# Performance work log

Measured on AMD Instinct MI355X. Metric: run time of the kernel, lower is better.

The kernel has to match this reference:

```python
import jax, jax.numpy as jnp
import numpy as np

# Dimensions
B, C, H, W, M, ND = 2, 16, 128, 128, 9, 9  # batch, feat, height, width, views, disparities
MC = M * C          # 144 channels after view stacking
HID = 18            # hidden channels in attention branches
OUT = 150           # output_dim of conv_last
EPS = 1e-5          # BatchNorm eps
PAD = 16            # max |d*(u-4)| = 4*4


def _conv3d(x, w, b, pad):
    # x: [N, Cin, D, H, W]; w: [Cout, Cin, kd, kh, kw]
    y = jax.lax.conv_general_dilated(
        x, w, window_strides=(1, 1, 1), padding=[(pad, pad)] * 3,
        dimension_numbers=('NCDHW', 'OIDHW', 'NCDHW'))
    return y + b.reshape(1, -1, 1, 1, 1)


def _bn(x, g, b, m, v):
    # eval-mode BatchNorm3d with running stats
    sh = (1, -1, 1, 1, 1)
    return (x - m.reshape(sh)) * (g * jax.lax.rsqrt(v + EPS)).reshape(sh) + b.reshape(sh)


def _cost_volume(x):
    # x: [B,C,H,W,M] -> cost volume [B,M,C,H,W,ND] (mode '0d': v=4, u=view index).
    # affine_grid(align_corners=False) theta=[[1,0,2d(u-4)/W],[0,1,0]] + bilinear
    # grid_sample is an EXACT integer horizontal shift: out[h,w] = in[h, w + d*(u-4)]
    # with zero padding outside the image.
    xv = jnp.transpose(x, (4, 0, 1, 2, 3))                      # [M,B,C,H,W]
    xp = jnp.pad(xv, ((0, 0), (0, 0), (0, 0), (PAD, PAD), (PAD, PAD)))
    vols = []
    for d in range(-4, 5):
        views = [xp[m, :, :, PAD:PAD + H, PAD + d * (m - 4):PAD + d * (m - 4) + W]
                 for m in range(M)]
        vols.append(jnp.stack(views, axis=1))                   # [B,M,C,H,W]
    return jnp.stack(vols, axis=-1)                             # [B,M,C,H,W,ND]


def setup_inputs() -> dict:
    key = jax.random.key(0)
    ks = jax.random.split(key, 32)
    f = lambda k, shape, s=0.05: (jax.random.normal(k, shape, jnp.float32) * s)
    inp = {
        'x': jax.random.normal(ks[0], (B, C, H, W, M), jnp.float32),
        # local attention branch
        'la_w1': f(ks[1], (HID, MC, 3, 3, 3)), 'la_b1': f(ks[2], (HID,)),
        'la_g1': 1.0 + f(ks[3], (HID,)), 'la_beta1': f(ks[4], (HID,)),
        'la_m1': f(ks[5], (HID,)), 'la_v1': 1.0 + 0.1 * jax.random.uniform(ks[6], (HID,), jnp.float32),
        'la_w2': f(ks[7], (M, HID, 3, 3, 3)), 'la_b2': f(ks[8], (M,)),
        'la_g2': 1.0 + f(ks[9], (M,)), 'la_beta2': f(ks[10], (M,)),
        'la_m2': f(ks[11], (M,)), 'la_v2': 1.0 + 0.1 * jax.random.uniform(ks[12], (M,), jnp.float32),
        # global attention branch
        'ga_w1': f(ks[13], (HID, MC, 3, 3, 3)), 'ga_b1': f(ks[14], (HID,)),
        'ga_g1': 1.0 + f(ks[15], (HID,)), 'ga_beta1': f(ks[16], (HID,)),
        'ga_m1': f(ks[17], (HID,)), 'ga_v1': 1.0 + 0.1 * jax.random.uniform(ks[18], (HID,), jnp.float32),
        'ga_w2': f(ks[19], (M, HID, 3, 3, 3)), 'ga_b2': f(ks[20], (M,)),
        'ga_g2': 1.0 + f(ks[21], (M,)), 'ga_beta2': f(ks[22], (M,)),
        'ga_m2': f(ks[23], (M,)), 'ga_v2': 1.0 + 0.1 * jax.random.uniform(ks[24], (M,), jnp.float32),
        # conv_last (1x1x1)
        'cl_w': f(ks[25], (OUT, MC, 1, 1, 1)), 'cl_b': f(ks[26], (OUT,)),
    }
    return inp


def reference(x, la_w1, la_b1, la_g1, la_beta1, la_m1, la_v1,
              la_w2, la_b2, la_g2, la_beta2, la_m2, la_v2,
              ga_w1, ga_b1, ga_g1, ga_beta1, ga_m1, ga_v1,
              ga_w2, ga_b2, ga_g2, ga_beta2, ga_m2, ga_v2,
              cl_w, cl_b):
    cv = _cost_volume(x)                                        # [B,M,C,H,W,ND]
    xr = cv.reshape(B, MC, H, W, ND)                            # [B,144,H,W,9]
    # local attention
    h = jax.nn.relu(_bn(_conv3d(xr, la_w1, la_b1, 1), la_g1, la_beta1, la_m1, la_v1))
    x_l = _bn(_conv3d(h, la_w2, la_b2, 1), la_g2, la_beta2, la_m2, la_v2)   # [B,9,H,W,9]
    # global attention (adaptive avg pool to 1x1x1 then same conv stack)
    p = jnp.mean(xr, axis=(2, 3, 4), keepdims=True)             # [B,144,1,1,1]
    g = jax.nn.relu(_bn(_conv3d(p, ga_w1, ga_b1, 1), ga_g1, ga_beta1, ga_m1, ga_v1))
    x_g = _bn(_conv3d(g, ga_w2, ga_b2, 1), ga_g2, ga_beta2, ga_m2, ga_v2)   # [B,9,1,1,1]
    wei = jax.nn.sigmoid(x_l + x_g).reshape(B, M, 1, H, W, ND)
    out = _conv3d((wei * cv).reshape(B, MC, H, W, ND), cl_w, cl_b, 0)       # [B,150,H,W,9]
    return out.reshape(B, -1, H, W, ND)
```

## Files before the change

kernel.cpp:

```cpp
#include <hip/hip_runtime.h>
#include <hip/hip_bf16.h>
#include <cstddef>

#define B_ 2
#define C_ 16
#define H_ 128
#define W_ 128
#define M_ 9
#define ND_ 9
#define MC_ 144
#define HID_ 18
#define OUT_ 150
#define GOC_ 152
#define EPS_ 1e-5f

#define OFF_P     0
#define OFF_XG    512
#define OFF_W1F   1024
#define OFF_B1F   71040
#define OFF_W2F   71104
#define OFF_B2F   75520
#define OFF_CLWT  75584
#define OFF_F     98304
#define OFF_HBUF  18069504
#define OFF_WEI   23377920
#define OFF_GB_BYTES (98304ull*4ull)

__global__ __launch_bounds__(256) void k_pool(const float* __restrict__ x,
                                              float* __restrict__ ws) {
  int bid = blockIdx.x;
  int z   = blockIdx.y;
  int b = bid / MC_, mc = bid % MC_;
  int m = mc / C_, c = mc % C_;
  int sm = m - 4;
  const float* xb = x + (size_t)(b*C_ + c)*H_*W_*M_;
  float acc = 0.f;
  int i0 = z * (H_*W_*ND_/8);
  int i1 = i0 + (H_*W_*ND_/8);
  for (int idx = i0 + (int)threadIdx.x; idx < i1; idx += 256) {
    int w = idx & 127;
    int t = idx >> 7;
    int d = t % 9;
    int h = t / 9;
    int wc = w + (d - 4)*sm;
    if (wc >= 0 && wc < W_) acc += xb[(h*W_ + wc)*M_ + m];
  }
  __shared__ float red[256];
  red[threadIdx.x] = acc;
  __syncthreads();
  for (int s = 128; s > 0; s >>= 1) {
    if ((int)threadIdx.x < s) red[threadIdx.x] += red[threadIdx.x + s];
    __syncthreads();
  }
  if (threadIdx.x == 0)
    atomicAdd(&ws[OFF_P + b*MC_ + mc], red[0] * (1.f/(float)(H_*W_*ND_)));
}

__global__ __launch_bounds__(256) void k_repack(
    const float* __restrict__ w1, const float* __restrict__ b1,
    const float* __restrict__ g1, const float* __restrict__ be1,
    const float* __restrict__ m1, const float* __restrict__ v1,
    const float* __restrict__ w2, const float* __restrict__ b2,
    const float* __restrict__ g2, const float* __restrict__ be2,
    const float* __restrict__ m2, const float* __restrict__ v2,
    const float* __restrict__ clw, float* __restrict__ ws) {
  int id = blockIdx.x*256 + threadIdx.x;
  if (id < 69984) {
    int o   = id % 18;
    int kdd = (id/18) % 3;
    int kh  = (id/54) % 3;
    int kw  = (id/162) % 3;
    int mc  = id/486;
    float s = g1[o] / sqrtf(v1[o] + EPS_);
    ws[OFF_W1F + id] = w1[(o*MC_ + mc)*27 + kh*9 + kw*3 + kdd] * s;
    return;
  }
  id -= 69984;
  if (id < 18) {
    float s = g1[id]/sqrtf(v1[id]+EPS_);
    ws[OFF_B1F + id] = (b1[id]-m1[id])*s + be1[id];
    return;
  }
  id -= 18;
  if (id < 4374) {
    int i = id % 9, tap = (id/9) % 27, c = id/243;
    float s = g2[i]/sqrtf(v2[i]+EPS_);
    ws[OFF_W2F + id] = w2[(i*HID_ + c)*27 + tap] * s;
    return;
  }
  id -= 4374;
  if (id < 9) {
    float s = g2[id]/sqrtf(v2[id]+EPS_);
    ws[OFF_B2F + id] = (b2[id]-m2[id])*s + be2[id];
    return;
  }
  id -= 9;
  if (id < 21600) {
    int oc = id % OUT_, mc = id / OUT_;
    ws[OFF_CLWT + id] = clw[oc*MC_ + mc];
  }
}

__global__ __launch_bounds__(64) void k_ga(
    const float* __restrict__ gw1, const float* __restrict__ gb1,
    const float* __restrict__ gg1, const float* __restrict__ gbe1,
    const float* __restrict__ gm1, const float* __restrict__ gv1,
    const float* __restrict__ gw2, const float* __restrict__ gb2,
    const float* __restrict__ gg2, const float* __restrict__ gbe2,
    const float* __restrict__ gm2, const float* __restrict__ gv2,
    float* __restrict__ ws) {
  __shared__ float gl[B_*HID_];
  int t = threadIdx.x;
  if (t < B_*HID_) {
    int b = t / HID_, j = t % HID_;
    float acc = gb1[j];
    for (int ch = 0; ch < MC_; ch++)
      acc += gw1[(j*MC_ + ch)*27 + 13] * ws[OFF_P + b*MC_ + ch];
    float s = gg1[j]/sqrtf(gv1[j]+EPS_);
    gl[t] = fmaxf((acc - gm1[j])*s + gbe1[j], 0.f);
  }
  __syncthreads();
  if (t < B_*M_) {
    int b = t / M_, i = t % M_;
    float acc = gb2[i];
    for (int j = 0; j < HID_; j++)
      acc += gw2[(i*HID_ + j)*27 + 13] * gl[b*HID_ + j];
    float s = gg2[i]/sqrtf(gv2[i]+EPS_);
    ws[OFF_XG + b*M_ + i] = (acc - gm2[i])*s + gbe2[i];
  }
}

__global__ __launch_bounds__(256) void k_F(const float* __restrict__ x,
                                           float* __restrict__ ws) {
  int h0 = blockIdx.x * 4;
  int m  = blockIdx.y;
  int b  = blockIdx.z;
  __shared__ float xt[C_*132*6];
  for (int e = threadIdx.x; e < C_*132*6; e += 256) {
    int hh = e % 6;
    int cc = (e/6) % 132;
    int c  = e / 792;
    int row = h0 - 1 + hh;
    int col = cc - 2;
    float v = 0.f;
    if (row >= 0 && row < H_ && col >= 0 && col < W_)
      v = x[(((size_t)(b*C_ + c)*H_ + row)*W_ + col)*M_ + m];
    xt[e] = v;
  }
  __syncthreads();
  const float* w1f = ws + OFF_W1F;
  float* Fb = ws + OFF_F + (size_t)(b*M_ + m)*3*H_*130*20;
  for (int pp = threadIdx.x; pp < 130*18; pp += 256) {
    int o   = pp % 18;
    int wpp = pp / 18;
    float acc[3][4] = {};
    for (int c = 0; c < C_; c++) {
      int wb = (m*C_ + c)*486 + o;
      #pragma unroll
      for (int kw = 0; kw < 3; kw++) {
        const float* xp = xt + (c*132 + wpp + kw)*6;
        float xv[6];
        #pragma unroll
        for (int q = 0; q < 6; q++) xv[q] = xp[q];
        const float* wp = w1f + wb + kw*162;
        #pragma unroll
        for (int kh = 0; kh < 3; kh++)
          #pragma unroll
          for (int kdd = 0; kdd < 3; kdd++) {
            float wv = wp[kh*54 + kdd*18];
            #pragma unroll
            for (int hh = 0; hh < 4; hh++)
              acc[kdd][hh] += wv * xv[hh + kh];
          }
      }
    }
    #pragma unroll
    for (int kdd = 0; kdd < 3; kdd++)
      #pragma unroll
      for (int hh = 0; hh < 4; hh++)
        Fb[(((size_t)kdd*H_ + (h0+hh))*130 + wpp)*20 + o] = acc[kdd][hh];
  }
}

__global__ __launch_bounds__(576) void k_comb1(const float* __restrict__ x,
                                               float* __restrict__ ws) {
  const int h = blockIdx.x;
  const int b = blockIdx.y;
  const int t = threadIdx.x;
  const int d    = t >> 6;
  const int lane = t & 63;

  __shared__ float fs[3*2730];
  __shared__ float xe[7776];
  __shared__ float corr[9][2][18];

  const int iA = t, iB = t + 576, iC = t + 1152, iD = t + 1728;
  const bool vD = (iD < 1950);
  const int kA = iA/650, rA_ = iA%650;
  const int kB = iB/650, rB_ = iB%650;
  const int kC = iC/650, rC_ = iC%650;
  const int kD = vD ? iD/650 : 0, rD_ = vD ? iD%650 : 0;
  const int gA = kA*332800 + h*2600 + rA_*4;
  const int gB = kB*332800 + h*2600 + rB_*4;
  const int gC = kC*332800 + h*2600 + rC_*4;
  const int gD = kD*332800 + h*2600 + rD_*4;
  const int lA = kA*2730 + (rA_/5)*21 + (rA_%5)*4;
  const int lB = kB*2730 + (rB_/5)*21 + (rB_%5)*4;
  const int lC = kC*2730 + (rC_/5)*21 + (rC_%5)*4;
  const int lD = kD*2730 + (rD_/5)*21 + (rD_%5)*4;

  size_t mb = (size_t)OFF_F + (size_t)(b*9 + 0)*998400;
  float4 rA = *(const float4*)(ws + mb + gA);
  float4 rB = *(const float4*)(ws + mb + gB);
  float4 rC = *(const float4*)(ws + mb + gC);
  float4 rD = vD ? *(const float4*)(ws + mb + gD) : make_float4(0.f,0.f,0.f,0.f);

  for (int e = t; e < 7776; e += 576) {
    int c    = e & 15;
    int kh   = (e >> 4) % 3;
    int dp   = (e / 48) % 9;
    int edge = (e / 432) & 1;
    int m    = e / 864;
    int row = h + kh - 1;
    int col = edge ? 128 + (dp - 4)*(m - 4) : (dp - 4)*(m - 4) - 1;
    float v = 0.f;
    if ((unsigned)row < 128u && (unsigned)col < 128u)
      v = x[(((size_t)(b*C_ + c)*H_ + row)*W_ + col)*M_ + m];
    xe[e] = v;
  }
  __syncthreads();

  if (t < 324) {
    int o    = t % 18;
    int edge = (t / 18) & 1;
    int dd   = t / 36;
    int kwe  = edge ? 2 : 0;
    const float* w1b = ws + OFF_W1F + kwe*162 + o;
    float s = 0.f;
    for (int m = 0; m < 9; m++) {
      #pragma unroll
      for (int kdd = 0; kdd < 3; kdd++) {
        int dp = dd + kdd - 1;
        if (dp < 0 || dp >= 9) continue;
        const float* xp = xe + ((m*2 + edge)*9 + dp)*48;
        const float* wp = w1b + m*7776 + kdd*18;
        for (int c = 0; c < 16; c++) {
          #pragma unroll
          for (int kh = 0; kh < 3; kh++)
            s += wp[c*486 + kh*54] * xp[kh*16 + c];
        }
      }
    }
    corr[dd][edge][o] = s;
  }

  float acc0[18], acc1[18];
  #pragma unroll
  for (int o = 0; o < 18; o++) {
    float bz = ws[OFF_B1F + o];
    acc0[o] = bz; acc1[o] = bz;
  }

  __syncthreads();

  for (int m = 0; m < 9; m++) {
    fs[lA+0]=rA.x; fs[lA+1]=rA.y; fs[lA+2]=rA.z; fs[lA+3]=rA.w;
    fs[lB+0]=rB.x; fs[lB+1]=rB.y; fs[lB+2]=rB.z; fs[lB+3]=rB.w;
    fs[lC+0]=rC.x; fs[lC+1]=rC.y; fs[lC+2]=rC.z; fs[lC+3]=rC.w;
    if (vD) { fs[lD+0]=rD.x; fs[lD+1]=rD.y; fs[lD+2]=rD.z; fs[lD+3]=rD.w; }
    if (m < 8) {
      mb = (size_t)OFF_F + (size_t)(b*9 + m + 1)*998400;
      rA = *(const float4*)(ws + mb + gA);
      rB = *(const float4*)(ws + mb + gB);
      rC = *(const float4*)(ws + mb + gC);
      if (vD) rD = *(const float4*)(ws + mb + gD);
    }
    __syncthreads();

    const int sm = m - 4;
    #pragma unroll
    for (int kdd = 0; kdd < 3; kdd++) {
      int dp = d + kdd - 1;
      if (dp >= 0 && dp < 9) {
        int shift = (dp - 4)*sm;
        const float* row_ = fs + kdd*2730;
        int wg0 = lane + shift;
        if (wg0 >= -1 && wg0 <= 128) {
          const float* p = row_ + (wg0 + 1)*21;
          #pragma unroll
          for (int o = 0; o < 18; o++) acc0[o] += p[o];
        }
        int wg1 = wg0 + 64;
        if (wg1 >= -1 && wg1 <= 128) {
          const float* p = row_ + (wg1 + 1)*21;
          #pragma unroll
          for (int o = 0; o < 18; o++) acc1[o] += p[o];
        }
      }
    }
    __syncthreads();
  }

  if (lane == 0) {
    #pragma unroll
    for (int o = 0; o < 18; o++) acc0[o] -= corr[d][0][o];
  }
  if (lane == 63) {
    #pragma unroll
    for (int o = 0; o < 18; o++) acc1[o] -= corr[d][1][o];
  }

  float* hb = ws + OFF_HBUF + ((size_t)((b*H_ + h)*ND_ + d)*W_)*18;
  float2* p0 = (float2*)(hb + (size_t)lane*18);
  float2* p1 = (float2*)(hb + (size_t)(lane + 64)*18);
  #pragma unroll
  for (int q = 0; q < 9; q++) {
    p0[q] = make_float2(fmaxf(acc0[2*q], 0.f), fmaxf(acc0[2*q+1], 0.f));
    p1[q] = make_float2(fmaxf(acc1[2*q], 0.f), fmaxf(acc1[2*q+1], 0.f));
  }
}

__global__ __launch_bounds__(576) void k_conv2(float* __restrict__ ws) {
  int w0 = blockIdx.x * 8;
  int h0 = blockIdx.y * 8;
  int b  = blockIdx.z;
  int t  = threadIdx.x;
  int lh = t / 72;
  int lw = (t / 9) % 8;
  int d  = t % 9;
  __shared__ float ht[9900];
  const float* hbuf = ws + OFF_HBUF;
  const float* w2f  = ws + OFF_W2F;
  float acc[9] = {};
  for (int c0 = 0; c0 < 18; c0 += 9) {
    __syncthreads();
    for (int e = t; e < 9900; e += 576) {
      int cc = e % 9;
      int dd = (e/9) % 11;
      int ww = (e/99) % 10;
      int hh = e / 990;
      int gh = h0 - 1 + hh, gw = w0 - 1 + ww, gd = dd - 1;
      float v = 0.f;
      if (gh >= 0 && gh < H_ && gw >= 0 && gw < W_ && gd >= 0 && gd < ND_)
        v = hbuf[(((size_t)(b*H_ + gh)*ND_ + gd)*W_ + gw)*18 + c0 + cc];
      ht[e] = v;
    }
    __syncthreads();
    for (int cc = 0; cc < 9; cc++) {
      #pragma unroll
      for (int kh = 0; kh < 3; kh++)
        #pragma unroll
        for (int kw = 0; kw < 3; kw++)
          #pragma unroll
          for (int kdd = 0; kdd < 3; kdd++) {
            float v = ht[(((lh+kh)*10 + (lw+kw))*11 + (d+kdd))*9 + cc];
            const float* wp = w2f + ((c0+cc)*27 + kh*9 + kw*3 + kdd)*9;
            #pragma unroll
            for (int i = 0; i < 9; i++) acc[i] += wp[i] * v;
          }
    }
  }
  int h = h0 + lh, w = w0 + lw;
  float* wei = ws + OFF_WEI + ((size_t)((b*H_ + h)*W_ + w)*9 + d)*9;
  const float* xg = ws + OFF_XG + b*M_;
  #pragma unroll
  for (int i = 0; i < 9; i++) {
    float y = acc[i] + ws[OFF_B2F + i] + xg[i];
    wei[i] = 1.f / (1.f + expf(-y));
  }
}

__global__ __launch_bounds__(192) void k_G(const float* __restrict__ x,
                                           const float* __restrict__ ws,
                                           __hip_bfloat16* __restrict__ Gb) {
  int h = blockIdx.x, m = blockIdx.y, b = blockIdx.z;
  __shared__ float xs[C_][W_];
  for (int e = threadIdx.x; e < C_*W_; e += 192) {
    int c = e >> 7, wp = e & 127;
    xs[c][wp] = x[(((size_t)(b*C_ + c)*H_ + h)*W_ + wp)*M_ + m];
  }
  __syncthreads();
  int oc = threadIdx.x;
  if (oc >= GOC_) return;
  __hip_bfloat16* Gr = Gb + ((size_t)(b*H_ + h)*M_ + m)*W_*GOC_;
  if (oc >= OUT_) {
    for (int wp = 0; wp < W_; wp++) Gr[wp*GOC_ + oc] = __float2bfloat16(0.f);
    return;
  }
  const float* clwT = ws + OFF_CLWT;
  float wreg[C_];
  #pragma unroll
  for (int c = 0; c < C_; c++) wreg[c] = clwT[(m*C_ + c)*OUT_ + oc];
  for (int wp0 = 0; wp0 < W_; wp0 += 4) {
    float a0 = 0.f, a1 = 0.f, a2 = 0.f, a3 = 0.f;
    #pragma unroll
    for (int c = 0; c < C_; c++) {
      float4 xv = *(const float4*)&xs[c][wp0];
      a0 += wreg[c]*xv.x; a1 += wreg[c]*xv.y;
      a2 += wreg[c]*xv.z; a3 += wreg[c]*xv.w;
    }
    Gr[(wp0+0)*GOC_ + oc] = __float2bfloat16(a0);
    Gr[(wp0+1)*GOC_ + oc] = __float2bfloat16(a1);
    Gr[(wp0+2)*GOC_ + oc] = __float2bfloat16(a2);
    Gr[(wp0+3)*GOC_ + oc] = __float2bfloat16(a3);
  }
}

__global__ __launch_bounds__(256) void k_last(const float* __restrict__ ws,
                                              const __hip_bfloat16* __restrict__ Gb,
                                              const float* __restrict__ clb,
                                              float* __restrict__ out) {
  int h = blockIdx.y;
  int b = blockIdx.z;
  int idx = blockIdx.x*256 + threadIdx.x;
  int w   = idx / 38;
  int ocq = idx % 38;
  int oc0 = ocq * 4;

  float acc[9][4];
  #pragma unroll
  for (int j = 0; j < 4; j++) {
    float cb = (oc0 + j < OUT_) ? clb[oc0 + j] : 0.f;
    #pragma unroll
    for (int d = 0; d < 9; d++) acc[d][j] = cb;
  }

  const float* wv = ws + OFF_WEI + (size_t)((b*H_ + h)*W_ + w)*81;
  const __hip_bfloat16* Gh = Gb + (size_t)(b*H_ + h)*M_*W_*GOC_;
  for (int m = 0; m < 9; m++) {
    int sm = m - 4;
    const __hip_bfloat16* Gm = Gh + (size_t)m*W_*GOC_;
    #pragma unroll
    for (int d = 0; d < 9; d++) {
      int wg = w + (d - 4)*sm;
      if (wg < 0 || wg >= W_) continue;
      ushort4 u = *(const ushort4*)(Gm + wg*GOC_ + oc0);
      float wf = wv[d*9 + m];
      acc[d][0] += wf * __uint_as_float(((unsigned)u.x) << 16);
      acc[d][1] += wf * __uint_as_float(((unsigned)u.y) << 16);
      acc[d][2] += wf * __uint_as_float(((unsigned)u.z) << 16);
      acc[d][3] += wf * __uint_as_float(((unsigned)u.w) << 16);
    }
  }

  #pragma unroll
  for (int j = 0; j < 4; j++) {
    int oc = oc0 + j;
    if (oc >= OUT_) break;
    float* op = out + (((size_t)(b*OUT_ + oc)*H_ + h)*W_ + w)*9;
    #pragma unroll
    for (int d = 0; d < 9; d++) op[d] = acc[d][j];
  }
}

extern "C" void kernel_launch(void* const* d_in, const int* in_sizes, int n_in,
                              void* d_out, int out_size, void* d_ws, size_t ws_size,
                              hipStream_t stream) {
  const float* x       = (const float*)d_in[0];
  const float* la_w1   = (const float*)d_in[1];
  const float* la_b1   = (const float*)d_in[2];
  const float* la_g1   = (const float*)d_in[3];
  const float* la_be1  = (const float*)d_in[4];
  const float* la_m1   = (const float*)d_in[5];
  const float* la_v1   = (const float*)d_in[6];
  const float* la_w2   = (const float*)d_in[7];
  const float* la_b2   = (const float*)d_in[8];
  const float* la_g2   = (const float*)d_in[9];
  const float* la_be2  = (const float*)d_in[10];
  const float* la_m2   = (const float*)d_in[11];
  const float* la_v2   = (const float*)d_in[12];
  const float* ga_w1   = (const float*)d_in[13];
  const float* ga_b1   = (const float*)d_in[14];
  const float* ga_g1   = (const float*)d_in[15];
  const float* ga_be1  = (const float*)d_in[16];
  const float* ga_m1   = (const float*)d_in[17];
  const float* ga_v1   = (const float*)d_in[18];
  const float* ga_w2   = (const float*)d_in[19];
  const float* ga_b2   = (const float*)d_in[20];
  const float* ga_g2   = (const float*)d_in[21];
  const float* ga_be2  = (const float*)d_in[22];
  const float* ga_m2   = (const float*)d_in[23];
  const float* ga_v2   = (const float*)d_in[24];
  const float* cl_w    = (const float*)d_in[25];
  const float* cl_b    = (const float*)d_in[26];

  float* ws = (float*)d_ws;
  __hip_bfloat16* Gb = (__hip_bfloat16*)((char*)d_ws + OFF_GB_BYTES);
  float* out = (float*)d_out;

  hipMemsetAsync(d_ws, 0, MC_*B_*sizeof(float), stream);
  k_pool  <<<dim3(288, 8), 256, 0, stream>>>(x, ws);
  k_repack<<<375, 256, 0, stream>>>(la_w1, la_b1, la_g1, la_be1, la_m1, la_v1,
                                    la_w2, la_b2, la_g2, la_be2, la_m2, la_v2,
                                    cl_w, ws);
  k_ga    <<<1, 64, 0, stream>>>(ga_w1, ga_b1, ga_g1, ga_be1, ga_m1, ga_v1,
                                 ga_w2, ga_b2, ga_g2, ga_be2, ga_m2, ga_v2, ws);
  k_F     <<<dim3(32, 9, 2), 256, 0, stream>>>(x, ws);
  k_comb1 <<<dim3(128, 2), 576, 0, stream>>>(x, ws);
  k_conv2 <<<dim3(16, 16, 2), 576, 0, stream>>>(ws);
  k_G     <<<dim3(128, 9, 2), 192, 0, stream>>>(x, ws, Gb);
  k_last  <<<dim3(19, 128, 2), 256, 0, stream>>>(ws, Gb, cl_b, out);
}
```

Measured before the change: 886.8 us.

## Stage k_F weights in shared memory and register-block five width positions per thread

k_F now loads the per-view first-conv weight slab into shared memory, and each thread keeps its 27 taps for an output channel in registers. Each thread computes five width positions for that channel, using 576 threads per block. The input tile is padded to 8 floats per column so it can be read with float4/float2 vector loads. This is meant to cut repeated global weight loads and scalar LDS traffic in exchange for higher register pressure, which may lower occupancy or cause spills.

```diff
diff --git a/kernel.cpp b/kernel.cpp
--- a/kernel.cpp
+++ b/kernel.cpp
@@ -130,55 +130,82 @@
   }
 }
 
-__global__ __launch_bounds__(256) void k_F(const float* __restrict__ x,
+__global__ __launch_bounds__(576) void k_F(const float* __restrict__ x,
                                            float* __restrict__ ws) {
   int h0 = blockIdx.x * 4;
   int m  = blockIdx.y;
   int b  = blockIdx.z;
-  __shared__ float xt[C_*132*6];
-  for (int e = threadIdx.x; e < C_*132*6; e += 256) {
+  const int t = threadIdx.x;
+  __shared__ float xt[C_*132*8];
+  __shared__ float wt[7776];
+  for (int e = t; e < 7776; e += 576)
+    wt[e] = ws[OFF_W1F + m*7776 + e];
+  for (int e = t; e < C_*132*6; e += 576) {
     int hh = e % 6;
     int cc = (e/6) % 132;
     int c  = e / 792;
     int row = h0 - 1 + hh;
     int col = cc - 2;
     float v = 0.f;
-    if (row >= 0 && row < H_ && col >= 0 && col < W_)
+    if ((unsigned)row < 128u && (unsigned)col < 128u)
       v = x[(((size_t)(b*C_ + c)*H_ + row)*W_ + col)*M_ + m];
-    xt[e] = v;
+    xt[(c*132 + cc)*8 + hh] = v;
   }
   __syncthreads();
-  const float* w1f = ws + OFF_W1F;
+
+  const int o  = t % 18;
+  const int wq = t / 18;
+  float acc[3][4][5];
+  #pragma unroll
+  for (int kdd = 0; kdd < 3; kdd++)
+    #pragma unroll
+    for (int hh = 0; hh < 4; hh++)
+      #pragma unroll
+      for (int p = 0; p < 5; p++) acc[kdd][hh][p] = 0.f;
+
+  for (int c = 0; c < C_; c++) {
+    float wreg[27];
+    #pragma unroll
+    for (int tap = 0; tap < 27; tap++) wreg[tap] = wt[c*486 + tap*18 + o];
+    #pragma unroll
+    for (int p = 0; p < 5; p++) {
+      int wpp = wq + p*32;
+      if (wpp < 130) {
+        const float* xb = &xt[(c*132 + wpp)*8];
+        float xv[3][6];
+        #pragma unroll
+        for (int kw = 0; kw < 3; kw++) {
+          float4 lo = *(const float4*)(xb + kw*8);
+          float2 hi = *(const float2*)(xb + kw*8 + 4);
+          xv[kw][0] = lo.x; xv[kw][1] = lo.y; xv[kw][2] = lo.z;
+          xv[kw][3] = lo.w; xv[kw][4] = hi.x; xv[kw][5] = hi.y;
+        }
+        #pragma unroll
+        for (int kw = 0; kw < 3; kw++)
+          #pragma unroll
+          for (int kh = 0; kh < 3; kh++)
+            #pragma unroll
+            for (int kdd = 0; kdd < 3; kdd++) {
+              float wv = wreg[kw*9 + kh*3 + kdd];
+              #pragma unroll
+              for (int hh = 0; hh < 4; hh++)
+                acc[kdd][hh][p] += wv * xv[kw][hh + kh];
+            }
+      }
+    }
+  }
+
   float* Fb = ws + OFF_F + (size_t)(b*M_ + m)*3*H_*130*20;
-  for (int pp = threadIdx.x; pp < 130*18; pp += 256) {
-    int o   = pp % 18;
-    int wpp = pp / 18;
-    float acc[3][4] = {};
-    for (int c = 0; c < C_; c++) {
-      int wb = (m*C_ + c)*486 + o;
+  #pragma unroll
+  for (int p = 0; p < 5; p++) {
+    int wpp = wq + p*32;
+    if (wpp < 130) {
       #pragma unroll
-      for (int kw = 0; kw < 3; kw++) {
-        const float* xp = xt + (c*132 + wpp + kw)*6;
-        float xv[6];
+      for (int kdd = 0; kdd < 3; kdd++)
         #pragma unroll
-        for (int q = 0; q < 6; q++) xv[q] = xp[q];
-        const float* wp = w1f + wb + kw*162;
-        #pragma unroll
-        for (int kh = 0; kh < 3; kh++)
-          #pragma unroll
-          for (int kdd = 0; kdd < 3; kdd++) {
-            float wv = wp[kh*54 + kdd*18];
-            #pragma unroll
-            for (int hh = 0; hh < 4; hh++)
-              acc[kdd][hh] += wv * xv[hh + kh];
-          }
-      }
-    }
-    #pragma unroll
-    for (int kdd = 0; kdd < 3; kdd++)
-      #pragma unroll
-      for (int hh = 0; hh < 4; hh++)
-        Fb[(((size_t)kdd*H_ + (h0+hh))*130 + wpp)*20 + o] = acc[kdd][hh];
+        for (int hh = 0; hh < 4; hh++)
+          Fb[(((size_t)kdd*H_ + (h0+hh))*130 + wpp)*20 + o] = acc[kdd][hh][p];
+    }
   }
 }
 
@@ -495,7 +522,7 @@
                                     cl_w, ws);
   k_ga    <<<1, 64, 0, stream>>>(ga_w1, ga_b1, ga_g1, ga_be1, ga_m1, ga_v1,
                                  ga_w2, ga_b2, ga_g2, ga_be2, ga_m2, ga_v2, ws);
-  k_F     <<<dim3(32, 9, 2), 256, 0, stream>>>(x, ws);
+  k_F     <<<dim3(32, 9, 2), 576, 0, stream>>>(x, ws);
   k_comb1 <<<dim3(128, 2), 576, 0, stream>>>(x, ws);
   k_conv2 <<<dim3(16, 16, 2), 576, 0, stream>>>(ws);
   k_G     <<<dim3(128, 9, 2), 192, 0, stream>>>(x, ws, Gb);
```

After: 965.4 us. 8.9% more time.

## Restructure first-conv F kernel with wave-uniform channels and register weights

Applied to the files above, without the earlier changes.

The weight-scaling kernel now writes a second copy of the first local-attention conv weights, laid out per view, output channel and input channel with the 27 taps contiguous. That copy sits in the tail of the hidden-activation buffer region, which is written later in the stream. The F kernel then gives each wave one output channel at a time, so weights are loaded uniformly into 27 registers per input channel. Each lane computes two width columns and reads shared memory with vector loads. A small tail path handles the last two padded columns. This removes repeated per-thread weight loads and the modulo-18 thread mapping, at the cost of more registers, and it relies on the float4 shared-memory reads at 24-byte strides being acceptable.

```diff
diff --git a/kernel.cpp b/kernel.cpp
--- a/kernel.cpp
+++ b/kernel.cpp
@@ -24,6 +24,7 @@
 #define OFF_F     98304
 #define OFF_HBUF  18069504
 #define OFF_WEI   23377920
+#define OFF_W1T   23307936
 #define OFF_GB_BYTES (98304ull*4ull)
 
 __global__ __launch_bounds__(256) void k_pool(const float* __restrict__ x,
@@ -98,6 +99,19 @@
   if (id < 21600) {
     int oc = id % OUT_, mc = id / OUT_;
     ws[OFF_CLWT + id] = clw[oc*MC_ + mc];
+    return;
+  }
+  id -= 21600;
+  if (id < 69984) {
+    int tap = id % 27;
+    int kw  = tap / 9;
+    int kh  = (tap % 9) / 3;
+    int kdd = tap % 3;
+    int c   = (id/27) % 16;
+    int o   = (id/432) % 18;
+    int m   = id / 7776;
+    float s = g1[o] / sqrtf(v1[o] + EPS_);
+    ws[OFF_W1T + id] = w1[(o*MC_ + m*C_ + c)*27 + kh*9 + kw*3 + kdd] * s;
   }
 }
 
@@ -135,39 +149,94 @@
   int h0 = blockIdx.x * 4;
   int m  = blockIdx.y;
   int b  = blockIdx.z;
+  const int t = threadIdx.x;
   __shared__ float xt[C_*132*6];
-  for (int e = threadIdx.x; e < C_*132*6; e += 256) {
+  for (int e = t; e < C_*132*6; e += 256) {
     int hh = e % 6;
     int cc = (e/6) % 132;
     int c  = e / 792;
     int row = h0 - 1 + hh;
     int col = cc - 2;
     float v = 0.f;
-    if (row >= 0 && row < H_ && col >= 0 && col < W_)
+    if ((unsigned)row < 128u && (unsigned)col < 128u)
       v = x[(((size_t)(b*C_ + c)*H_ + row)*W_ + col)*M_ + m];
     xt[e] = v;
   }
   __syncthreads();
-  const float* w1f = ws + OFF_W1F;
+
+  const int wave = __builtin_amdgcn_readfirstlane(t >> 6);
+  const int lane = t & 63;
+  const float* w1t = ws + OFF_W1T + (size_t)m*7776;
   float* Fb = ws + OFF_F + (size_t)(b*M_ + m)*3*H_*130*20;
-  for (int pp = threadIdx.x; pp < 130*18; pp += 256) {
-    int o   = pp % 18;
-    int wpp = pp / 18;
-    float acc[3][4] = {};
+
+  for (int oi = 0; oi < 5; oi++) {
+    int o = wave + oi*4;
+    if (o >= 18) break;
+    float acc[3][4][2];
+    #pragma unroll
+    for (int kdd = 0; kdd < 3; kdd++)
+      #pragma unroll
+      for (int hh = 0; hh < 4; hh++) {
+        acc[kdd][hh][0] = 0.f; acc[kdd][hh][1] = 0.f;
+      }
     for (int c = 0; c < C_; c++) {
-      int wb = (m*C_ + c)*486 + o;
+      const float* wp = w1t + (o*16 + c)*27;
+      float wreg[27];
+      #pragma unroll
+      for (int i = 0; i < 27; i++) wreg[i] = wp[i];
+      #pragma unroll
+      for (int wq = 0; wq < 2; wq++) {
+        int wpp = wq*64 + lane;
+        #pragma unroll
+        for (int kw = 0; kw < 3; kw++) {
+          const float* xb = &xt[(c*132 + wpp + kw)*6];
+          float4 lo = *(const float4*)xb;
+          float2 hi = *(const float2*)(xb + 4);
+          float xv[6] = {lo.x, lo.y, lo.z, lo.w, hi.x, hi.y};
+          #pragma unroll
+          for (int kh = 0; kh < 3; kh++)
+            #pragma unroll
+            for (int kdd = 0; kdd < 3; kdd++) {
+              float wv = wreg[kw*9 + kh*3 + kdd];
+              #pragma unroll
+              for (int hh = 0; hh < 4; hh++)
+                acc[kdd][hh][wq] += wv * xv[hh + kh];
+            }
+        }
+      }
+    }
+    #pragma unroll
+    for (int wq = 0; wq < 2; wq++) {
+      int wpp = wq*64 + lane;
+      #pragma unroll
+      for (int kdd = 0; kdd < 3; kdd++)
+        #pragma unroll
+        for (int hh = 0; hh < 4; hh++)
+          Fb[(((size_t)kdd*H_ + (h0+hh))*130 + wpp)*20 + o] = acc[kdd][hh][wq];
+    }
+  }
+
+  if (t < 36) {
+    int o   = t % 18;
+    int wpp = 128 + t/18;
+    float acc[3][4];
+    #pragma unroll
+    for (int kdd = 0; kdd < 3; kdd++)
+      #pragma unroll
+      for (int hh = 0; hh < 4; hh++) acc[kdd][hh] = 0.f;
+    for (int c = 0; c < C_; c++) {
+      const float* wp = w1t + (o*16 + c)*27;
       #pragma unroll
       for (int kw = 0; kw < 3; kw++) {
-        const float* xp = xt + (c*132 + wpp + kw)*6;
-        float xv[6];
-        #pragma unroll
-        for (int q = 0; q < 6; q++) xv[q] = xp[q];
-        const float* wp = w1f + wb + kw*162;
+        const float* xb = &xt[(c*132 + wpp + kw)*6];
+        float4 lo = *(const float4*)xb;
+        float2 hi = *(const float2*)(xb + 4);
+        float xv[6] = {lo.x, lo.y, lo.z, lo.w, hi.x, hi.y};
         #pragma unroll
         for (int kh = 0; kh < 3; kh++)
           #pragma unroll
           for (int kdd = 0; kdd < 3; kdd++) {
-            float wv = wp[kh*54 + kdd*18];
+            float wv = wp[kw*9 + kh*3 + kdd];
             #pragma unroll
             for (int hh = 0; hh < 4; hh++)
               acc[kdd][hh] += wv * xv[hh + kh];
@@ -490,7 +559,7 @@
 
   hipMemsetAsync(d_ws, 0, MC_*B_*sizeof(float), stream);
   k_pool  <<<dim3(288, 8), 256, 0, stream>>>(x, ws);
-  k_repack<<<375, 256, 0, stream>>>(la_w1, la_b1, la_g1, la_be1, la_m1, la_v1,
+  k_repack<<<649, 256, 0, stream>>>(la_w1, la_b1, la_g1, la_be1, la_m1, la_v1,
                                     la_w2, la_b2, la_g2, la_be2, la_m2, la_v2,
                                     cl_w, ws);
   k_ga    <<<1, 64, 0, stream>>>(ga_w1, ga_b1, ga_g1, ga_be1, ga_m1, ga_v1,
```

New measurement: 915.9 us. 3.3% more time.
